# Performance work log

Measured on AMD Instinct MI355X. Metric: run time of the kernel, lower is better.

The kernel has to match this reference:

```python
import jax, jax.numpy as jnp
import numpy as np

N_EMBD = 256
N_INPUTS = 66
N_LEVELS = 8
AND_PER_LEVEL = 4096
NOT_PER_LEVEL = 2048
LEVEL = AND_PER_LEVEL + NOT_PER_LEVEL
N_NODES = N_INPUTS + N_LEVELS * LEVEL  # 49218
N_HIDDEN = 4 * N_EMBD  # 1024
N_HID_LAYERS = 8
LN_EPS = 1e-5


def setup_inputs() -> dict:
    rng = np.random.default_rng(0)
    nodes = np.zeros(N_NODES, dtype=np.int32)
    x_edges = np.zeros(N_NODES, dtype=np.int32)
    y_edges = np.zeros(N_NODES, dtype=np.int32)
    for l in range(N_LEVELS):
        s = N_INPUTS + l * LEVEL
        nodes[s:s + AND_PER_LEVEL] = 1           # AND gates
        nodes[s + AND_PER_LEVEL:s + LEVEL] = 2   # NOT gates
        # predecessors strictly earlier in topological order -> valid DAG
        x_edges[s:s + LEVEL] = rng.integers(0, s, LEVEL)
        y_edges[s:s + LEVEL] = rng.integers(0, s, LEVEL)

    key = jax.random.key(0)
    ks = jax.random.split(key, 5)
    s_in = 1.0 / np.sqrt(2 * N_EMBD)
    s_h = 1.0 / np.sqrt(N_HIDDEN)
    return {
        "nodes": jnp.asarray(nodes),
        "x_edges": jnp.asarray(x_edges),
        "y_edges": jnp.asarray(y_edges),
        "input_embd": jax.random.uniform(ks[0], (N_INPUTS, N_EMBD), jnp.float32, -1.0, 1.0),
        "W_in": jax.random.normal(ks[1], (2 * N_EMBD, N_HIDDEN), jnp.float32) * s_in,
        "b_in": jnp.zeros((N_HIDDEN,), jnp.float32),
        "W_hid": jax.random.normal(ks[2], (N_HID_LAYERS, N_HIDDEN, N_HIDDEN), jnp.float32) * s_h,
        "b_hid": jnp.zeros((N_HID_LAYERS, N_HIDDEN), jnp.float32),
        "W_out": jax.random.normal(ks[3], (N_HIDDEN, N_EMBD), jnp.float32) * s_h,
        "b_out": jnp.zeros((N_EMBD,), jnp.float32),
        "ln_g": jnp.ones((N_EMBD,), jnp.float32),
        "ln_b": jnp.zeros((N_EMBD,), jnp.float32),
    }


def _layernorm(x, g, b):
    mu = jnp.mean(x, axis=-1, keepdims=True)
    var = jnp.var(x, axis=-1, keepdims=True)
    return (x - mu) * jax.lax.rsqrt(var + LN_EPS) * g + b


def _mlp(x, W_in, b_in, W_hid, b_hid, W_out, b_out):
    h = jax.nn.relu(x @ W_in + b_in)
    for i in range(N_HID_LAYERS):
        h = jax.nn.relu(h @ W_hid[i] + b_hid[i])
    return h @ W_out + b_out  # dropout p=0.05 is identity in eval mode


def reference(nodes, x_edges, y_edges, input_embd, W_in, b_in, W_hid, b_hid,
              W_out, b_out, ln_g, ln_b):
    # node_embd: [N_NODES, N_EMBD]; input nodes seeded, rest zero
    node_embd = jnp.zeros((N_NODES, N_EMBD), input_embd.dtype).at[:N_INPUTS].set(input_embd)
    # topological wavefronts == contiguous levels in this DAG layout; the torch
    # while-loop processes exactly these sets (order over levels is forced by
    # the x_ready/y_ready dependency tracking), so a static level loop is exact.
    for l in range(N_LEVELS):
        s = N_INPUTS + l * LEVEL
        # NOT gates: negate x-predecessor embedding (processed first, as in torch)
        xn = x_edges[s + AND_PER_LEVEL:s + LEVEL]
        node_embd = node_embd.at[s + AND_PER_LEVEL:s + LEVEL].set(-node_embd[xn])
        # AND gates: LayerNorm(MLP(concat(x_pred, y_pred)))
        xa = x_edges[s:s + AND_PER_LEVEL]
        ya = y_edges[s:s + AND_PER_LEVEL]
        h = jnp.concatenate([node_embd[xa], node_embd[ya]], axis=-1)  # [A, 512]
        out = _layernorm(_mlp(h, W_in, b_in, W_hid, b_hid, W_out, b_out), ln_g, ln_b)
        node_embd = node_embd.at[s:s + AND_PER_LEVEL].set(out)
    return node_embd
```

## Files before the change

### kernel.cpp

```cpp
#include <hip/hip_runtime.h>
#include <hip/hip_bf16.h>
#include <stdint.h>

#define N_EMBD    256
#define N_INPUTS  66
#define N_LEVELS  8
#define APL       4096
#define NPL       2048
#define LVL       6144
#define N_HID     1024

typedef __hip_bfloat16 bf16;
typedef __attribute__((ext_vector_type(8))) short short8;
typedef __attribute__((ext_vector_type(4))) float f32x4;

static __device__ __forceinline__ unsigned short f2b(float f) {
  bf16 h = __float2bfloat16(f);
  return *reinterpret_cast<unsigned short*>(&h);
}

__global__ void k_copy_inputs(const float* __restrict__ in, float* __restrict__ out) {
  int r = blockIdx.x, t = threadIdx.x;
  ((float4*)(out + (size_t)r * 256))[t] = ((const float4*)(in + (size_t)r * 256))[t];
}

__global__ void k_transpose_all(const float* __restrict__ W_in, const float* __restrict__ W_hid,
                                const float* __restrict__ W_out,
                                bf16* __restrict__ WtIn, bf16* __restrict__ WtHid,
                                bf16* __restrict__ WtOut) {
  __shared__ float t[32][33];
  int z = blockIdx.z;
  const float* in; bf16* out; int K, N;
  if (z == 0)      { in = W_in;  out = WtIn;  K = 512;  N = 1024; }
  else if (z <= 8) { in = W_hid + (size_t)(z - 1) * 1024 * 1024; out = WtHid + (size_t)(z - 1) * 1024 * 1024; K = 1024; N = 1024; }
  else             { in = W_out; out = WtOut; K = 1024; N = 256; }
  int n0 = blockIdx.x * 32, k0 = blockIdx.y * 32;
  if (n0 >= N || k0 >= K) return;
  int tx = threadIdx.x, ty = threadIdx.y;
  #pragma unroll
  for (int j = 0; j < 32; j += 8)
    t[ty + j][tx] = in[(size_t)(k0 + ty + j) * N + n0 + tx];
  __syncthreads();
  #pragma unroll
  for (int j = 0; j < 32; j += 8)
    out[(size_t)(n0 + ty + j) * K + k0 + tx] = __float2bfloat16(t[tx][ty + j]);
}

__global__ void k_not_gather(const int* __restrict__ xe, const int* __restrict__ ye,
                             float* __restrict__ node, bf16* __restrict__ H0, int s) {
  int t = threadIdx.x & 63;
  int b = blockIdx.x * 4 + (threadIdx.x >> 6);
  if (b < NPL) {
    int dst = s + APL + b;
    int src = xe[dst];
    float4 v = ((const float4*)(node + (size_t)src * 256))[t];
    float4 o; o.x = -v.x; o.y = -v.y; o.z = -v.z; o.w = -v.w;
    ((float4*)(node + (size_t)dst * 256))[t] = o;
  } else {
    int r = b - NPL;
    int xa = xe[s + r], ya = ye[s + r];
    float4 vx = ((const float4*)(node + (size_t)xa * 256))[t];
    float4 vy = ((const float4*)(node + (size_t)ya * 256))[t];
    ushort4 ox, oy;
    ox.x = f2b(vx.x); ox.y = f2b(vx.y); ox.z = f2b(vx.z); ox.w = f2b(vx.w);
    oy.x = f2b(vy.x); oy.y = f2b(vy.y); oy.z = f2b(vy.z); oy.w = f2b(vy.w);
    bf16* hr = H0 + (size_t)r * 512;
    ((ushort4*)hr)[t] = ox;
    ((ushort4*)(hr + 256))[t] = oy;
  }
}

template<int BM, int BN, int NK, bool RELU, bool BF16OUT>
__global__ __launch_bounds__(256, 2)
void k_gemm(const bf16* __restrict__ A, const bf16* __restrict__ Bt,
            const float* __restrict__ bias, void* __restrict__ Cout,
            int M, int N, int K) {
  constexpr int MT = BM / 32;
  constexpr int NT = BN / 32;
  constexpr int AIT = BM / 32;
  constexpr int BIT = BN / 32;
  constexpr int ABYTES = BM * 128;
  constexpr int BBYTES = BN * 128;
  constexpr int BUF = ABYTES + BBYTES;
  constexpr int LOADS = AIT + BIT;
  __shared__ __align__(16) char smem[3 * BUF];

  const int tid  = threadIdx.x;
  const int lane = tid & 63;
  const int w    = tid >> 6;
  const int wm   = w >> 1, wn = w & 1;
  const int m0 = blockIdx.x * BM;
  const int n0 = blockIdx.y * BN;

  const bf16* gA[AIT];
  const bf16* gB[BIT];
  #pragma unroll
  for (int it = 0; it < AIT; ++it) {
    int ci = it * 256 + tid;
    int r = ci >> 3, g = ci & 7, gs = g ^ (r & 7);
    gA[it] = A + (size_t)(m0 + r) * K + gs * 8;
  }
  #pragma unroll
  for (int it = 0; it < BIT; ++it) {
    int ci = it * 256 + tid;
    int r = ci >> 3, g = ci & 7, gs = g ^ (r & 7);
    gB[it] = Bt + (size_t)(n0 + r) * K + gs * 8;
  }

  int aoff[2][MT], boff[2][NT];
  #pragma unroll
  for (int kk = 0; kk < 2; ++kk) {
    #pragma unroll
    for (int mt = 0; mt < MT; ++mt) {
      int row = wm * (BM / 2) + mt * 16 + (lane & 15);
      int g = kk * 4 + (lane >> 4);
      aoff[kk][mt] = row * 128 + ((g ^ (row & 7)) * 16);
    }
    #pragma unroll
    for (int nt = 0; nt < NT; ++nt) {
      int row = wn * (BN / 2) + nt * 16 + (lane & 15);
      int g = kk * 4 + (lane >> 4);
      boff[kk][nt] = ABYTES + row * 128 + ((g ^ (row & 7)) * 16);
    }
  }

  f32x4 acc[MT][NT] = {};

  auto STAGE = [&](char* base) {
    char* sA = base;
    char* sB = base + ABYTES;
    #pragma unroll
    for (int it = 0; it < AIT; ++it) {
      __builtin_amdgcn_global_load_lds((const __attribute__((address_space(1))) void*)gA[it],
                                       (__attribute__((address_space(3))) void*)(sA + (it * 256 + w * 64) * 16),
                                       16, 0, 0);
      gA[it] += 64;
    }
    #pragma unroll
    for (int it = 0; it < BIT; ++it) {
      __builtin_amdgcn_global_load_lds((const __attribute__((address_space(1))) void*)gB[it],
                                       (__attribute__((address_space(3))) void*)(sB + (it * 256 + w * 64) * 16),
                                       16, 0, 0);
      gB[it] += 64;
    }
  };

  auto COMPUTE = [&](char* base) {
    #pragma unroll
    for (int kk = 0; kk < 2; ++kk) {
      short8 af[MT], bfr[NT];
      #pragma unroll
      for (int mt = 0; mt < MT; ++mt)
        af[mt] = *(const short8*)(base + aoff[kk][mt]);
      #pragma unroll
      for (int nt = 0; nt < NT; ++nt)
        bfr[nt] = *(const short8*)(base + boff[kk][nt]);
      #pragma unroll
      for (int mt = 0; mt < MT; ++mt)
        #pragma unroll
        for (int nt = 0; nt < NT; ++nt)
          acc[mt][nt] = __builtin_amdgcn_mfma_f32_16x16x32_bf16(af[mt], bfr[nt], acc[mt][nt], 0, 0, 0);
    }
  };

  STAGE(smem);
  STAGE(smem + BUF);

  #pragma unroll
  for (int t = 0; t < NK; ++t) {
    if (t < NK - 1) {
      if constexpr (LOADS == 6)      asm volatile("s_waitcnt vmcnt(6)" ::: "memory");
      else if constexpr (LOADS == 4) asm volatile("s_waitcnt vmcnt(4)" ::: "memory");
      else                           asm volatile("s_waitcnt vmcnt(0)" ::: "memory");
    } else {
      asm volatile("s_waitcnt vmcnt(0)" ::: "memory");
    }
    __builtin_amdgcn_s_barrier();
    if (t + 2 < NK) STAGE(smem + ((t + 2) % 3) * BUF);
    COMPUTE(smem + (t % 3) * BUF);
  }

  #pragma unroll
  for (int nt = 0; nt < NT; ++nt) {
    int col = n0 + wn * (BN / 2) + nt * 16 + (lane & 15);
    float bv = bias[col];
    #pragma unroll
    for (int mt = 0; mt < MT; ++mt) {
      int rbase = m0 + wm * (BM / 2) + mt * 16 + (lane >> 4) * 4;
      #pragma unroll
      for (int r = 0; r < 4; ++r) {
        float v = acc[mt][nt][r] + bv;
        if (RELU) v = fmaxf(v, 0.f);
        if (BF16OUT)
          ((unsigned short*)Cout)[(size_t)(rbase + r) * N + col] = f2b(v);
        else
          ((float*)Cout)[(size_t)(rbase + r) * N + col] = v;
      }
    }
  }
}

__global__ void k_ln(const float* __restrict__ X, const float* __restrict__ g,
                     const float* __restrict__ b, float* __restrict__ node, int s) {
  int t = threadIdx.x & 63;
  int r = blockIdx.x * 4 + (threadIdx.x >> 6);
  float4 x = ((const float4*)(X + (size_t)r * 256))[t];
  float sm = x.x + x.y + x.z + x.w;
  float sq = x.x * x.x + x.y * x.y + x.z * x.z + x.w * x.w;
  #pragma unroll
  for (int o = 1; o < 64; o <<= 1) { sm += __shfl_xor(sm, o); sq += __shfl_xor(sq, o); }
  float mu  = sm * (1.f / 256.f);
  float var = sq * (1.f / 256.f) - mu * mu;
  float rs  = rsqrtf(var + 1e-5f);
  float4 gv = ((const float4*)g)[t], bv = ((const float4*)b)[t];
  float4 o4;
  o4.x = (x.x - mu) * rs * gv.x + bv.x;
  o4.y = (x.y - mu) * rs * gv.y + bv.y;
  o4.z = (x.z - mu) * rs * gv.z + bv.z;
  o4.w = (x.w - mu) * rs * gv.w + bv.w;
  ((float4*)(node + (size_t)(s + r) * 256))[t] = o4;
}

extern "C" void kernel_launch(void* const* d_in, const int* in_sizes, int n_in,
                              void* d_out, int out_size, void* d_ws, size_t ws_size,
                              hipStream_t stream) {
  const int*   x_edges    = (const int*)d_in[1];
  const int*   y_edges    = (const int*)d_in[2];
  const float* input_embd = (const float*)d_in[3];
  const float* W_in       = (const float*)d_in[4];
  const float* b_in       = (const float*)d_in[5];
  const float* W_hid      = (const float*)d_in[6];
  const float* b_hid      = (const float*)d_in[7];
  const float* W_out      = (const float*)d_in[8];
  const float* b_out      = (const float*)d_in[9];
  const float* ln_g       = (const float*)d_in[10];
  const float* ln_b       = (const float*)d_in[11];
  float* node = (float*)d_out;

  char* ws = (char*)d_ws;
  bf16* WtIn  = (bf16*)(ws);
  bf16* WtHid = (bf16*)(ws + (size_t)1048576);
  bf16* WtOut = (bf16*)(ws + (size_t)17825792);
  bf16* H0    = (bf16*)(ws + (size_t)18350080);
  bf16* HA    = (bf16*)(ws + (size_t)22544384);
  bf16* HB    = (bf16*)(ws + (size_t)30932992);
  float* OutF = (float*)HB;

  k_copy_inputs<<<dim3(66), dim3(64), 0, stream>>>(input_embd, node);

  k_transpose_all<<<dim3(32, 32, 10), dim3(32, 8), 0, stream>>>(W_in, W_hid, W_out, WtIn, WtHid, WtOut);

  for (int l = 0; l < N_LEVELS; ++l) {
    int s = N_INPUTS + l * LVL;
    k_not_gather<<<dim3((NPL + APL) / 4), dim3(256), 0, stream>>>(x_edges, y_edges, node, H0, s);

    k_gemm<128, 64, 8, true, true><<<dim3(32, 16), dim3(256), 0, stream>>>(H0, WtIn, b_in, HA, 4096, 1024, 512);
    const bf16* src = HA; bf16* dst = HB;
    for (int i = 0; i < 8; ++i) {
      k_gemm<128, 64, 16, true, true><<<dim3(32, 16), dim3(256), 0, stream>>>(
          src, WtHid + (size_t)i * 1024 * 1024, b_hid + i * 1024, dst, 4096, 1024, 1024);
      const bf16* tmp = src; src = dst; dst = (bf16*)tmp;
    }
    k_gemm<64, 64, 16, false, false><<<dim3(64, 4), dim3(256), 0, stream>>>(src, WtOut, b_out, OutF, 4096, 256, 1024);

    k_ln<<<dim3(APL / 4), dim3(256), 0, stream>>>(OutF, ln_g, ln_b, node, s);
  }
}
```

Baseline: 942.6 us.

## Fuse output projection GEMM with LayerNorm epilogue into one kernel

```diff
diff --git a/kernel.cpp b/kernel.cpp
--- a/kernel.cpp
+++ b/kernel.cpp
@@ -200,25 +200,143 @@
   }
 }
 
-__global__ void k_ln(const float* __restrict__ X, const float* __restrict__ g,
-                     const float* __restrict__ b, float* __restrict__ node, int s) {
-  int t = threadIdx.x & 63;
-  int r = blockIdx.x * 4 + (threadIdx.x >> 6);
-  float4 x = ((const float4*)(X + (size_t)r * 256))[t];
-  float sm = x.x + x.y + x.z + x.w;
-  float sq = x.x * x.x + x.y * x.y + x.z * x.z + x.w * x.w;
-  #pragma unroll
-  for (int o = 1; o < 64; o <<= 1) { sm += __shfl_xor(sm, o); sq += __shfl_xor(sq, o); }
-  float mu  = sm * (1.f / 256.f);
-  float var = sq * (1.f / 256.f) - mu * mu;
-  float rs  = rsqrtf(var + 1e-5f);
-  float4 gv = ((const float4*)g)[t], bv = ((const float4*)b)[t];
-  float4 o4;
-  o4.x = (x.x - mu) * rs * gv.x + bv.x;
-  o4.y = (x.y - mu) * rs * gv.y + bv.y;
-  o4.z = (x.z - mu) * rs * gv.z + bv.z;
-  o4.w = (x.w - mu) * rs * gv.w + bv.w;
-  ((float4*)(node + (size_t)(s + r) * 256))[t] = o4;
+__global__ __launch_bounds__(256, 1)
+void k_gemm_out_ln(const bf16* __restrict__ A, const bf16* __restrict__ Bt,
+                   const float* __restrict__ bias, const float* __restrict__ g,
+                   const float* __restrict__ b, float* __restrict__ node,
+                   int s, int K) {
+  constexpr int NK = 16;
+  constexpr int MT = 4, NT = 4, AIT = 2, BIT = 8;
+  constexpr int ABYTES = 64 * 128;
+  constexpr int BBYTES = 256 * 128;
+  constexpr int BUF = ABYTES + BBYTES;
+  __shared__ __align__(16) char smem[3 * BUF];
+  float* cls = (float*)smem;
+
+  const int tid  = threadIdx.x;
+  const int lane = tid & 63;
+  const int w    = tid >> 6;
+  const int m0 = blockIdx.x * 64;
+
+  const bf16* gA[AIT];
+  const bf16* gB[BIT];
+  #pragma unroll
+  for (int it = 0; it < AIT; ++it) {
+    int ci = it * 256 + tid;
+    int r = ci >> 3, gg = ci & 7, gs = gg ^ (r & 7);
+    gA[it] = A + (size_t)(m0 + r) * K + gs * 8;
+  }
+  #pragma unroll
+  for (int it = 0; it < BIT; ++it) {
+    int ci = it * 256 + tid;
+    int r = ci >> 3, gg = ci & 7, gs = gg ^ (r & 7);
+    gB[it] = Bt + (size_t)r * K + gs * 8;
+  }
+
+  int aoff[2][MT], boff[2][NT];
+  #pragma unroll
+  for (int kk = 0; kk < 2; ++kk) {
+    #pragma unroll
+    for (int mt = 0; mt < MT; ++mt) {
+      int row = mt * 16 + (lane & 15);
+      int gg = kk * 4 + (lane >> 4);
+      aoff[kk][mt] = row * 128 + ((gg ^ (row & 7)) * 16);
+    }
+    #pragma unroll
+    for (int nt = 0; nt < NT; ++nt) {
+      int row = w * 64 + nt * 16 + (lane & 15);
+      int gg = kk * 4 + (lane >> 4);
+      boff[kk][nt] = ABYTES + row * 128 + ((gg ^ (row & 7)) * 16);
+    }
+  }
+
+  f32x4 acc[MT][NT] = {};
+
+  auto STAGE = [&](char* base) {
+    char* sA = base;
+    char* sB = base + ABYTES;
+    #pragma unroll
+    for (int it = 0; it < AIT; ++it) {
+      __builtin_amdgcn_global_load_lds((const __attribute__((address_space(1))) void*)gA[it],
+                                       (__attribute__((address_space(3))) void*)(sA + (it * 256 + w * 64) * 16),
+                                       16, 0, 0);
+      gA[it] += 64;
+    }
+    #pragma unroll
+    for (int it = 0; it < BIT; ++it) {
+      __builtin_amdgcn_global_load_lds((const __attribute__((address_space(1))) void*)gB[it],
+                                       (__attribute__((address_space(3))) void*)(sB + (it * 256 + w * 64) * 16),
+                                       16, 0, 0);
+      gB[it] += 64;
+    }
+  };
+
+  auto COMPUTE = [&](char* base) {
+    #pragma unroll
+    for (int kk = 0; kk < 2; ++kk) {
+      short8 af[MT], bfr[NT];
+      #pragma unroll
+      for (int mt = 0; mt < MT; ++mt)
+        af[mt] = *(const short8*)(base + aoff[kk][mt]);
+      #pragma unroll
+      for (int nt = 0; nt < NT; ++nt)
+        bfr[nt] = *(const short8*)(base + boff[kk][nt]);
+      #pragma unroll
+      for (int mt = 0; mt < MT; ++mt)
+        #pragma unroll
+        for (int nt = 0; nt < NT; ++nt)
+          acc[mt][nt] = __builtin_amdgcn_mfma_f32_16x16x32_bf16(af[mt], bfr[nt], acc[mt][nt], 0, 0, 0);
+    }
+  };
+
+  STAGE(smem);
+  STAGE(smem + BUF);
+
+  #pragma unroll
+  for (int t = 0; t < NK; ++t) {
+    if (t < NK - 1) asm volatile("s_waitcnt vmcnt(10)" ::: "memory");
+    else            asm volatile("s_waitcnt vmcnt(0)" ::: "memory");
+    __builtin_amdgcn_s_barrier();
+    if (t + 2 < NK) STAGE(smem + ((t + 2) % 3) * BUF);
+    COMPUTE(smem + (t % 3) * BUF);
+  }
+
+  __syncthreads();
+
+  #pragma unroll
+  for (int nt = 0; nt < NT; ++nt) {
+    int col = w * 64 + nt * 16 + (lane & 15);
+    float bv = bias[col];
+    #pragma unroll
+    for (int mt = 0; mt < MT; ++mt) {
+      int rbase = mt * 16 + (lane >> 4) * 4;
+      #pragma unroll
+      for (int r = 0; r < 4; ++r)
+        cls[(size_t)(rbase + r) * 256 + col] = acc[mt][nt][r] + bv;
+    }
+  }
+  __syncthreads();
+
+  float4 gv = ((const float4*)g)[lane];
+  float4 bv4 = ((const float4*)b)[lane];
+  #pragma unroll
+  for (int rr = 0; rr < 16; ++rr) {
+    int row = w * 16 + rr;
+    float4 x = ((const float4*)(cls + (size_t)row * 256))[lane];
+    float sm = x.x + x.y + x.z + x.w;
+    float sq = x.x * x.x + x.y * x.y + x.z * x.z + x.w * x.w;
+    #pragma unroll
+    for (int o = 1; o < 64; o <<= 1) { sm += __shfl_xor(sm, o); sq += __shfl_xor(sq, o); }
+    float mu  = sm * (1.f / 256.f);
+    float var = sq * (1.f / 256.f) - mu * mu;
+    float rs  = rsqrtf(var + 1e-5f);
+    float4 o4;
+    o4.x = (x.x - mu) * rs * gv.x + bv4.x;
+    o4.y = (x.y - mu) * rs * gv.y + bv4.y;
+    o4.z = (x.z - mu) * rs * gv.z + bv4.z;
+    o4.w = (x.w - mu) * rs * gv.w + bv4.w;
+    ((float4*)(node + (size_t)(s + m0 + row) * 256))[lane] = o4;
+  }
 }
 
 extern "C" void kernel_launch(void* const* d_in, const int* in_sizes, int n_in,
@@ -244,7 +362,6 @@
   bf16* H0    = (bf16*)(ws + (size_t)18350080);
   bf16* HA    = (bf16*)(ws + (size_t)22544384);
   bf16* HB    = (bf16*)(ws + (size_t)30932992);
-  float* OutF = (float*)HB;
 
   k_copy_inputs<<<dim3(66), dim3(64), 0, stream>>>(input_embd, node);
 
@@ -261,8 +378,6 @@
           src, WtHid + (size_t)i * 1024 * 1024, b_hid + i * 1024, dst, 4096, 1024, 1024);
       const bf16* tmp = src; src = dst; dst = (bf16*)tmp;
     }
-    k_gemm<64, 64, 16, false, false><<<dim3(64, 4), dim3(256), 0, stream>>>(src, WtOut, b_out, OutF, 4096, 256, 1024);
-
-    k_ln<<<dim3(APL / 4), dim3(256), 0, stream>>>(OutF, ln_g, ln_b, node, s);
-  }
-}
+    k_gemm_out_ln<<<dim3(64), dim3(256), 0, stream>>>(src, WtOut, b_out, ln_g, ln_b, node, s, 1024);
+  }
+}
```

New measurement: 978.1 us. 1.04x slower.
